# Performance work log

Hardware: AMD Instinct MI355X
Metric: run time of the kernel (lower is better)

Reference implementation:

```python
import jax, jax.numpy as jnp
import numpy as np
from jax import lax

N_NODES = 16384
N_EDGES = 262144
T = 64
F_IN = 8
H1, C1 = 12, 16          # globals H and O in the source
HID2 = H1 * C1           # 192, input to second GATConv
LSTM_H = 128
TRAIN_LEN = 32
TARGET_ID = 0
NEG_SLOPE = 0.2


def setup_inputs() -> dict:
    key = jax.random.key(0)
    ks = jax.random.split(key, 16)
    x = jax.random.normal(ks[0], (T, N_NODES, F_IN), jnp.float32)
    src = jax.random.randint(ks[1], (T, N_EDGES), 0, N_NODES)
    dst = jax.random.randint(ks[2], (T, N_EDGES), 0, N_NODES)
    dst = jnp.where(dst == src, (dst + 1) % N_NODES, dst)  # guarantee no self-loops
    edge_index = jnp.stack([src, dst], axis=1)  # (T, 2, E)
    g = lambda k, sh: jax.random.normal(k, sh, jnp.float32) * 0.1
    return {
        "x": x, "edge_index": edge_index,
        "Wl1": g(ks[3], (F_IN, H1 * C1)),
        "att_l1": g(ks[4], (1, H1, C1)), "att_r1": g(ks[5], (1, H1, C1)),
        "b1": jnp.zeros((H1 * C1,), jnp.float32),
        "Wl2": g(ks[6], (HID2, 1)),
        "att_l2": g(ks[7], (1, 1, 1)), "att_r2": g(ks[8], (1, 1, 1)),
        "b2": jnp.zeros((1,), jnp.float32),
        "Wih0": g(ks[9], (4 * LSTM_H, 1)), "Whh0": g(ks[10], (4 * LSTM_H, LSTM_H)),
        "bih0": jnp.zeros((4 * LSTM_H,), jnp.float32), "bhh0": jnp.zeros((4 * LSTM_H,), jnp.float32),
        "Wih1": g(ks[11], (4 * LSTM_H, LSTM_H)), "Whh1": g(ks[12], (4 * LSTM_H, LSTM_H)),
        "bih1": jnp.zeros((4 * LSTM_H,), jnp.float32), "bhh1": jnp.zeros((4 * LSTM_H,), jnp.float32),
        "Wlin": g(ks[13], (1, LSTM_H)), "blin": jnp.zeros((1,), jnp.float32),
    }


def _gat(x, ei, W, att_l, att_r, b, heads, outc, concat):
    N = x.shape[0]
    xl = (x @ W).reshape(N, heads, outc)              # (N,H,C)
    al = jnp.sum(xl * att_l, axis=-1)                 # (N,H)
    ar = jnp.sum(xl * att_r, axis=-1)                 # (N,H)
    loop = jnp.arange(N)
    src = jnp.concatenate([ei[0], loop])              # add self loops (inputs have none)
    dst = jnp.concatenate([ei[1], loop])
    alpha = jax.nn.leaky_relu(al[src] + ar[dst], NEG_SLOPE)  # (E+N, H)
    # segment softmax over destination neighborhoods
    amax = jax.ops.segment_max(alpha, dst, num_segments=N)
    ex = jnp.exp(alpha - amax[dst])
    alpha = ex / (jax.ops.segment_sum(ex, dst, num_segments=N)[dst] + 1e-16)
    # hardcoded per-edge-row edits from message(): s and v copies, then blend
    s = alpha.at[jnp.array([1, 2, 12, 19, 22])].set(0.0).at[jnp.array([7, 14])].set(1.0)
    v = alpha.at[jnp.array([10, 13])].set(0.5).at[jnp.array([17])].set(0.0)
    alpha = 0.8 * alpha + 0.1 * s + 0.1 * v
    out = jax.ops.segment_sum(xl[src] * alpha[:, :, None], dst, num_segments=N)  # (N,H,C)
    out = out.reshape(N, heads * outc) if concat else out.mean(axis=1)
    return out + b


def _lstm_layer(xs, Wih, Whh, bih, bhh):
    # xs: (L, B, in) -> hs: (L, B, H); torch gate order i,f,g,o
    Bsz, Hd = xs.shape[1], Whh.shape[1]
    def step(carry, xt):
        h, c = carry
        gates = xt @ Wih.T + h @ Whh.T + bih + bhh
        i, f, g, o = jnp.split(gates, 4, axis=-1)
        c = jax.nn.sigmoid(f) * c + jax.nn.sigmoid(i) * jnp.tanh(g)
        h = jax.nn.sigmoid(o) * jnp.tanh(c)
        return (h, c), h
    init = (jnp.zeros((Bsz, Hd), xs.dtype), jnp.zeros((Bsz, Hd), xs.dtype))
    _, hs = lax.scan(step, init, xs)
    return hs


def reference(x, edge_index, Wl1, att_l1, att_r1, b1, Wl2, att_l2, att_r2, b2,
              Wih0, Whh0, bih0, bhh0, Wih1, Whh1, bih1, bhh1, Wlin, blin):
    def per_t(args):
        xt, eit = args
        h = _gat(xt, eit, Wl1, att_l1, att_r1, b1, H1, C1, True)
        h = jax.nn.elu(h)
        h = _gat(h, eit, Wl2, att_l2, att_r2, b2, 1, 1, False)
        return h[:, 0]
    out = lax.map(per_t, (x, edge_index))             # (T, N) == xs_out
    series = lax.stop_gradient(out[:, TARGET_ID])     # split_sequences detaches
    idx = jnp.arange(T - TRAIN_LEN)[:, None] + jnp.arange(TRAIN_LEN)[None, :]
    ts = series[idx][:, :, None]                      # (B, L, 1), batch_first
    xs = jnp.transpose(ts, (1, 0, 2))                 # (L, B, 1)
    hs = _lstm_layer(xs, Wih0, Whh0, bih0, bhh0)
    hs = _lstm_layer(hs, Wih1, Whh1, bih1, bhh1)
    return hs[-1] @ Wlin.T + blin                     # (B, 1)
```

## Files before the change

### kernel.cpp

```cpp
#include <hip/hip_runtime.h>
#include <math.h>

#define T 64
#define NN 16384
#define NE 262144
#define FIN 8
#define H1H 12
#define C1C 16
#define HID 192
#define CAP2 95
#define SCAP 96
#define DEGCAP 127
#define LH 128
#define G4 512
#define NB 32
#define NL 32

#define DEV __device__ __forceinline__

DEV float wave_max(float v){
  #pragma unroll
  for (int m = 32; m; m >>= 1) v = fmaxf(v, __shfl_xor(v, m));
  return v;
}
DEV float wave_sum(float v){
  #pragma unroll
  for (int m = 32; m; m >>= 1) v += __shfl_xor(v, m);
  return v;
}
DEV float leaky(float x){ return x >= 0.f ? x : 0.2f * x; }
DEV float sigmoidf(float x){ return 1.f / (1.f + expf(-x)); }

DEV float apply_edit(float a, int eid){
  if (eid >= 32) return a;
  const unsigned m09 = (1u<<1)|(1u<<2)|(1u<<7)|(1u<<10)|(1u<<12)|(1u<<13)|(1u<<14)|(1u<<17)|(1u<<19)|(1u<<22);
  const unsigned mp1 = (1u<<7)|(1u<<14);
  const unsigned mp05 = (1u<<10)|(1u<<13);
  unsigned b = 1u << eid;
  float r = (m09 & b) ? 0.9f * a : a;
  if (mp1 & b) r += 0.1f;
  if (mp05 & b) r += 0.05f;
  return r;
}

__global__ __launch_bounds__(256) void k_scan0(const int* __restrict__ ei,
                                               int* __restrict__ cnt2, int* __restrict__ list2){
  long long gid = (long long)blockIdx.x * blockDim.x + threadIdx.x;
  long long e4 = gid * 4;
  int t = (int)(e4 >> 18);
  int e = (int)(e4 & (NE - 1));
  const int* dstp = ei + (size_t)t * 2 * NE + NE + e;
  int4 d = *(const int4*)dstp;
  int dd[4] = {d.x, d.y, d.z, d.w};
  #pragma unroll
  for (int q = 0; q < 4; q++){
    if (dd[q] == 0){
      int pos = atomicAdd(&cnt2[t], 1);
      if (pos < CAP2) list2[t * CAP2 + pos] = e + q;
    }
  }
}

__global__ __launch_bounds__(128) void k_build(const int* __restrict__ ei, const int* __restrict__ cnt2,
                                               const int* __restrict__ list2, int* __restrict__ scnt,
                                               int* __restrict__ Slist, int* __restrict__ slot_of,
                                               int* __restrict__ wcnt, int* __restrict__ wlist){
  int t = blockIdx.x;
  int* so = slot_of + (size_t)t * NN;
  int m = min(cnt2[t], CAP2);
  for (int i = threadIdx.x; i < m + 1; i += blockDim.x){
    int u = (i == m) ? 0 : ei[(size_t)t * 2 * NE + list2[t * CAP2 + i]];
    int old = atomicCAS(&so[u], -1, -2);
    if (old == -1){
      int s = atomicAdd(&scnt[t], 1);
      Slist[t * SCAP + s] = u;
      int w = atomicAdd(wcnt, 1);
      wlist[w] = (t << 8) | s;
      __hip_atomic_store(&so[u], s, __ATOMIC_RELAXED, __HIP_MEMORY_SCOPE_AGENT);
    }
  }
}

__global__ __launch_bounds__(256) void k_scan1(const int* __restrict__ ei, const int* __restrict__ slot_of,
                                               int* __restrict__ ecnt1, int* __restrict__ elist1){
  long long gid = (long long)blockIdx.x * blockDim.x + threadIdx.x;
  long long e4 = gid * 4;
  int t = (int)(e4 >> 18);
  int e = (int)(e4 & (NE - 1));
  const int* dstp = ei + (size_t)t * 2 * NE + NE + e;
  int4 d = *(const int4*)dstp;
  int dd[4] = {d.x, d.y, d.z, d.w};
  #pragma unroll
  for (int q = 0; q < 4; q++){
    int sl = slot_of[(size_t)t * NN + dd[q]];
    if (sl >= 0){
      int pos = atomicAdd(&ecnt1[t * SCAP + sl], 1);
      if (pos < DEGCAP) elist1[((size_t)t * SCAP + sl) * DEGCAP + pos] = e + q;
    }
  }
}

__global__ __launch_bounds__(256, 4) void k_gat1(const float* __restrict__ x, const int* __restrict__ ei,
                                             const float* __restrict__ Wl1, const float* __restrict__ attl,
                                             const float* __restrict__ attr, const float* __restrict__ b1,
                                             const int* __restrict__ wcnt, const int* __restrict__ wlist,
                                             const int* __restrict__ Slist,
                                             const int* __restrict__ ecnt1, const int* __restrict__ elist1,
                                             float* __restrict__ h1){
  int lane = threadIdx.x & 63;
  int wid = blockIdx.x * (blockDim.x >> 6) + (threadIdx.x >> 6);
  int nwaves = gridDim.x * (blockDim.x >> 6);
  int ntask = wcnt[0] * H1H;

  for (int task = wid; task < ntask; task += nwaves){
    int pi = task / H1H;
    int h = task - pi * H1H;
    int pair = wlist[pi];
    int t = pair >> 8, s = pair & 255;

    int u = Slist[t * SCAP + s];
    int deg = min(ecnt1[t * SCAP + s], DEGCAP);
    int tot = deg + 1;
    bool two = tot > 64;
    const float* xt = x + (size_t)t * NN * FIN;
    const int* srcp = ei + (size_t)t * 2 * NE;
    const int* el = elist1 + ((size_t)t * SCAP + s) * DEGCAP;

    float4 xu_a = ((const float4*)(xt + (size_t)u * FIN))[0];
    float4 xu_b = ((const float4*)(xt + (size_t)u * FIN))[1];
    float xu[FIN] = {xu_a.x, xu_a.y, xu_a.z, xu_a.w, xu_b.x, xu_b.y, xu_b.z, xu_b.w};

    bool act0 = lane < tot;
    int eid0 = 1 << 29;
    int su0 = u;
    if (lane < deg){ int e = el[lane]; eid0 = e; su0 = srcp[e]; }
    float4 xs0a = ((const float4*)(xt + (size_t)su0 * FIN))[0];
    float4 xs0b = ((const float4*)(xt + (size_t)su0 * FIN))[1];
    float xsrc0[FIN] = {xs0a.x, xs0a.y, xs0a.z, xs0a.w, xs0b.x, xs0b.y, xs0b.z, xs0b.w};

    bool act1 = false; int eid1 = 1 << 29;
    float xsrc1[FIN];
    if (two){
      int idx = 64 + lane;
      act1 = idx < tot;
      int su1 = u;
      if (idx < deg){ int e = el[idx]; eid1 = e; su1 = srcp[e]; }
      float4 xs1a = ((const float4*)(xt + (size_t)su1 * FIN))[0];
      float4 xs1b = ((const float4*)(xt + (size_t)su1 * FIN))[1];
      #pragma unroll
      for (int f = 0; f < 4; f++) xsrc1[f] = (&xs1a.x)[f];
      #pragma unroll
      for (int f = 0; f < 4; f++) xsrc1[4 + f] = (&xs1b.x)[f];
    }

    const float* Wh = Wl1 + h * C1C;
    const float* attlh = attl + h * C1C;
    const float* attrh = attr + h * C1C;

    float ar = 0.f;
    #pragma unroll
    for (int c = 0; c < C1C; c++){
      float v = 0.f;
      #pragma unroll
      for (int f = 0; f < FIN; f++) v = fmaf(xu[f], Wh[f * HID + c], v);
      ar = fmaf(v, attrh[c], ar);
    }

    float xls0[C1C];
    float al0 = 0.f;
    #pragma unroll
    for (int c = 0; c < C1C; c++){
      float v = 0.f;
      #pragma unroll
      for (int f = 0; f < FIN; f++) v = fmaf(xsrc0[f], Wh[f * HID + c], v);
      xls0[c] = v;
      al0 = fmaf(v, attlh[c], al0);
    }
    float raw0 = act0 ? leaky(al0 + ar) : -INFINITY;

    float xls1[C1C];
    float raw1 = -INFINITY;
    if (two){
      float al1 = 0.f;
      #pragma unroll
      for (int c = 0; c < C1C; c++){
        float v = 0.f;
        #pragma unroll
        for (int f = 0; f < FIN; f++) v = fmaf(xsrc1[f], Wh[f * HID + c], v);
        xls1[c] = v;
        al1 = fmaf(v, attlh[c], al1);
      }
      raw1 = act1 ? leaky(al1 + ar) : -INFINITY;
    }

    float M = wave_max(fmaxf(raw0, raw1));
    float ex0 = act0 ? expf(raw0 - M) : 0.f;
    float ex1 = act1 ? expf(raw1 - M) : 0.f;
    float S = wave_sum(ex0 + ex1);
    float den = S + 1e-16f;
    float alpha0 = apply_edit(ex0 / den, eid0);
    float alpha1 = two ? apply_edit(ex1 / den, eid1) : 0.f;

    float sum[C1C];
    #pragma unroll
    for (int c = 0; c < C1C; c++){
      sum[c] = xls0[c] * alpha0;
      if (two) sum[c] = fmaf(xls1[c], alpha1, sum[c]);
    }
    #pragma unroll
    for (int m = 32; m; m >>= 1){
      #pragma unroll
      for (int c = 0; c < C1C; c++) sum[c] += __shfl_xor(sum[c], m);
    }
    if (lane == 0){
      float* h1p = h1 + ((size_t)t * SCAP + s) * HID + h * C1C;
      #pragma unroll
      for (int c = 0; c < C1C; c++){
        float v = sum[c] + b1[h * C1C + c];
        h1p[c] = v > 0.f ? v : expm1f(v);
      }
    }
  }
}

__global__ __launch_bounds__(64) void k_gat2(const int* __restrict__ ei, const float* __restrict__ Wl2,
                                             const float* __restrict__ attl2_, const float* __restrict__ attr2_,
                                             const float* __restrict__ b2, const int* __restrict__ cnt2,
                                             const int* __restrict__ list2, const int* __restrict__ slot_of,
                                             const float* __restrict__ h1, float* __restrict__ series){
  int t = blockIdx.x; int lane = threadIdx.x;
  int deg = min(cnt2[t], CAP2);
  int tot = deg + 1;
  const int* srcp = ei + (size_t)t * 2 * NE;
  const int* so = slot_of + (size_t)t * NN;
  float attl2 = attl2_[0], attr2 = attr2_[0];
  int sl0 = so[0];
  const float* h1t = h1 + (size_t)t * SCAP * HID;

  float x0 = 0.f;
  for (int k = 0; k < HID; k++) x0 += h1t[(size_t)sl0 * HID + k] * Wl2[k];

  bool act[2]; int eid[2]; float xl2[2];
  #pragma unroll
  for (int ch = 0; ch < 2; ch++){
    int idx = ch * 64 + lane;
    act[ch] = idx < tot;
    eid[ch] = 1 << 29;
    int sl = sl0;
    if (idx < deg){ int e = list2[t * CAP2 + idx]; eid[ch] = e; sl = so[srcp[e]]; }
    float v = 0.f;
    if (act[ch]) for (int k = 0; k < HID; k++) v += h1t[(size_t)sl * HID + k] * Wl2[k];
    xl2[ch] = v;
  }
  float raw[2];
  #pragma unroll
  for (int ch = 0; ch < 2; ch++) raw[ch] = act[ch] ? leaky(attl2 * xl2[ch] + attr2 * x0) : -INFINITY;
  float M = wave_max(fmaxf(raw[0], raw[1]));
  float ex[2];
  #pragma unroll
  for (int ch = 0; ch < 2; ch++) ex[ch] = act[ch] ? expf(raw[ch] - M) : 0.f;
  float S = wave_sum(ex[0] + ex[1]);
  float den = S + 1e-16f;
  float contrib = apply_edit(ex[0] / den, eid[0]) * xl2[0] + apply_edit(ex[1] / den, eid[1]) * xl2[1];
  contrib = wave_sum(contrib);
  if (lane == 0) series[t] = contrib + b2[0];
}

#define AT_LOADR(p)    __hip_atomic_load((p), __ATOMIC_RELAXED, __HIP_MEMORY_SCOPE_AGENT)
#define AT_STORER(p,v) __hip_atomic_store((p), (v), __ATOMIC_RELAXED, __HIP_MEMORY_SCOPE_AGENT)

#define REP16(M) M(0)M(1)M(2)M(3)M(4)M(5)M(6)M(7)M(8)M(9)M(10)M(11)M(12)M(13)M(14)M(15)
#define WDECL(i) float4 w##i;
#define WLOAD(i) w##i = Wr[i];
#define WPIN(i)  asm volatile("" : "+v"(w##i.x), "+v"(w##i.y), "+v"(w##i.z), "+v"(w##i.w));
#define WFMA(i)  { float4 hv = h4b[i]; a0 = fmaf(w##i.x, hv.x, a0); a1 = fmaf(w##i.y, hv.y, a1); \
                   a2 = fmaf(w##i.z, hv.z, a2); a3 = fmaf(w##i.w, hv.w, a3); }

__global__ __launch_bounds__(512, 2) void k_lstm(const float* __restrict__ series,
    const float* __restrict__ Wih0, const float* __restrict__ Whh0,
    const float* __restrict__ bih0, const float* __restrict__ bhh0,
    const float* __restrict__ Wih1, const float* __restrict__ Whh1,
    const float* __restrict__ bih1, const float* __restrict__ bhh1,
    const float* __restrict__ Wlin, const float* __restrict__ blin,
    float* __restrict__ h0g, float* __restrict__ xpart,
    int* __restrict__ flagA, int* __restrict__ flagB, float* __restrict__ out){
  int j = threadIdx.x;
  int st = blockIdx.x >> 5;
  int b = blockIdx.x & 31;
  __shared__ float4 Wt4[16 * 512];
  __shared__ __align__(16) float h_lds[LH];
  __shared__ float c_lds[LH];
  __shared__ float gate_lds[G4];
  __shared__ float s_series[NL];
  const float4* h4b = (const float4*)h_lds;

  const float* Wsrc = (st == 0) ? Whh0 : (st == 1) ? Wih1 : Whh1;
  const float4* Wr = (const float4*)(Wsrc + (size_t)j * LH);
  REP16(WDECL)
  REP16(WLOAD)
  REP16(WPIN)
  #pragma unroll
  for (int q = 0; q < 16; q++) Wt4[q * 512 + j] = Wr[16 + q];

  if (st == 0){
    float wih = Wih0[j];
    float bsum = bih0[j] + bhh0[j];
    if (j < LH){ h_lds[j] = 0.f; c_lds[j] = 0.f; }
    if (j < NL) s_series[j] = series[b + j];
    __syncthreads();
    for (int t = 0; t < NL; t++){
      float a0 = 0.f, a1 = 0.f, a2 = 0.f, a3 = 0.f;
      REP16(WFMA)
      #pragma unroll
      for (int q = 0; q < 16; q++){
        float4 hv = h4b[16 + q];
        float4 wv = Wt4[q * 512 + j];
        a0 = fmaf(wv.x, hv.x, a0); a1 = fmaf(wv.y, hv.y, a1);
        a2 = fmaf(wv.z, hv.z, a2); a3 = fmaf(wv.w, hv.w, a3);
      }
      gate_lds[j] = fmaf(wih, s_series[t], bsum) + (a0 + a1) + (a2 + a3);
      __syncthreads();
      if (j < LH){
        float ig = sigmoidf(gate_lds[j]);
        float fg = sigmoidf(gate_lds[LH + j]);
        float gg = tanhf(gate_lds[2 * LH + j]);
        float og = sigmoidf(gate_lds[3 * LH + j]);
        float c = fg * c_lds[j] + ig * gg;
        float h = og * tanhf(c);
        c_lds[j] = c; h_lds[j] = h;
        AT_STORER(&h0g[(b * NL + t) * LH + j], h);
      }
      __syncthreads();
      if (j == 0) AT_STORER(&flagA[b], t + 1);
    }
  } else if (st == 1){
    __syncthreads();
    for (int t = 0; t < NL; t++){
      if (j == 0){
        while (AT_LOADR(&flagA[b]) < t + 1) __builtin_amdgcn_s_sleep(1);
      }
      __syncthreads();
      if (j < LH) h_lds[j] = AT_LOADR(&h0g[(b * NL + t) * LH + j]);
      __syncthreads();
      float a0 = 0.f, a1 = 0.f, a2 = 0.f, a3 = 0.f;
      REP16(WFMA)
      #pragma unroll
      for (int q = 0; q < 16; q++){
        float4 hv = h4b[16 + q];
        float4 wv = Wt4[q * 512 + j];
        a0 = fmaf(wv.x, hv.x, a0); a1 = fmaf(wv.y, hv.y, a1);
        a2 = fmaf(wv.z, hv.z, a2); a3 = fmaf(wv.w, hv.w, a3);
      }
      AT_STORER(&xpart[(b * NL + t) * G4 + j], (a0 + a1) + (a2 + a3));
      __syncthreads();
      if (j == 0) AT_STORER(&flagB[b], t + 1);
    }
  } else {
    float bsum = bih1[j] + bhh1[j];
    if (j < LH){ h_lds[j] = 0.f; c_lds[j] = 0.f; }
    __syncthreads();
    for (int t = 0; t < NL; t++){
      if (j == 0){
        while (AT_LOADR(&flagB[b]) < t + 1) __builtin_amdgcn_s_sleep(1);
      }
      __syncthreads();
      float xj = AT_LOADR(&xpart[(b * NL + t) * G4 + j]);
      float a0 = 0.f, a1 = 0.f, a2 = 0.f, a3 = 0.f;
      REP16(WFMA)
      #pragma unroll
      for (int q = 0; q < 16; q++){
        float4 hv = h4b[16 + q];
        float4 wv = Wt4[q * 512 + j];
        a0 = fmaf(wv.x, hv.x, a0); a1 = fmaf(wv.y, hv.y, a1);
        a2 = fmaf(wv.z, hv.z, a2); a3 = fmaf(wv.w, hv.w, a3);
      }
      gate_lds[j] = xj + bsum + (a0 + a1) + (a2 + a3);
      __syncthreads();
      if (j < LH){
        float ig = sigmoidf(gate_lds[j]);
        float fg = sigmoidf(gate_lds[LH + j]);
        float gg = tanhf(gate_lds[2 * LH + j]);
        float og = sigmoidf(gate_lds[3 * LH + j]);
        float c = fg * c_lds[j] + ig * gg;
        float h = og * tanhf(c);
        c_lds[j] = c; h_lds[j] = h;
      }
      __syncthreads();
    }
    if (j == 0){
      float s2 = blin[0];
      for (int k = 0; k < LH; k++) s2 += Wlin[k] * h_lds[k];
      out[b] = s2;
    }
  }
}

extern "C" void kernel_launch(void* const* d_in, const int* in_sizes, int n_in,
                              void* d_out, int out_size, void* d_ws, size_t ws_size,
                              hipStream_t stream) {
  const float* x     = (const float*)d_in[0];
  const int*   ei    = (const int*)  d_in[1];
  const float* Wl1   = (const float*)d_in[2];
  const float* attl1 = (const float*)d_in[3];
  const float* attr1 = (const float*)d_in[4];
  const float* b1    = (const float*)d_in[5];
  const float* Wl2   = (const float*)d_in[6];
  const float* attl2 = (const float*)d_in[7];
  const float* attr2 = (const float*)d_in[8];
  const float* b2    = (const float*)d_in[9];
  const float* Wih0  = (const float*)d_in[10];
  const float* Whh0  = (const float*)d_in[11];
  const float* bih0  = (const float*)d_in[12];
  const float* bhh0  = (const float*)d_in[13];
  const float* Wih1  = (const float*)d_in[14];
  const float* Whh1  = (const float*)d_in[15];
  const float* bih1  = (const float*)d_in[16];
  const float* bhh1  = (const float*)d_in[17];
  const float* Wlin  = (const float*)d_in[18];
  const float* blin  = (const float*)d_in[19];
  float* out = (float*)d_out;

  char* wsb = (char*)d_ws;
  size_t off = 0;
  auto alloc = [&](size_t bytes)->void*{
    void* p = wsb + off;
    off += (bytes + 255) & ~(size_t)255;
    return p;
  };
  int* cnt2  = (int*)alloc(T * 4);
  int* scnt  = (int*)alloc(T * 4);
  int* ecnt1 = (int*)alloc(T * SCAP * 4);
  int* flagA = (int*)alloc(NB * 4);
  int* flagB = (int*)alloc(NB * 4);
  int* wcnt  = (int*)alloc(4);
  size_t ctrl_bytes = off;
  int* slot_of = (int*)alloc((size_t)T * NN * 4);
  int* list2   = (int*)alloc((size_t)T * CAP2 * 4);
  int* Slist   = (int*)alloc((size_t)T * SCAP * 4);
  int* wlist   = (int*)alloc((size_t)T * SCAP * 4);
  int* elist1  = (int*)alloc((size_t)T * SCAP * DEGCAP * 4);
  float* h1    = (float*)alloc((size_t)T * SCAP * HID * 4);
  float* series= (float*)alloc(T * 4);
  float* h0g   = (float*)alloc((size_t)NB * NL * LH * 4);
  float* xpart = (float*)alloc((size_t)NB * NL * G4 * 4);

  hipMemsetAsync(d_ws, 0, ctrl_bytes, stream);
  hipMemsetAsync(slot_of, 0xFF, (size_t)T * NN * 4, stream);

  k_scan0<<<T * NE / 4 / 256, 256, 0, stream>>>(ei, cnt2, list2);
  k_build<<<T, 128, 0, stream>>>(ei, cnt2, list2, scnt, Slist, slot_of, wcnt, wlist);
  k_scan1<<<T * NE / 4 / 256, 256, 0, stream>>>(ei, slot_of, ecnt1, elist1);
  k_gat1<<<512, 256, 0, stream>>>(x, ei, Wl1, attl1, attr1, b1, wcnt, wlist, Slist, ecnt1, elist1, h1);
  k_gat2<<<T, 64, 0, stream>>>(ei, Wl2, attl2, attr2, b2, cnt2, list2, slot_of, h1, series);
  k_lstm<<<96, 512, 0, stream>>>(series, Wih0, Whh0, bih0, bhh0, Wih1, Whh1, bih1, bhh1,
                                 Wlin, blin, h0g, xpart, flagA, flagB, out);
}
```

Measured before the change: 495.2 us.

## Fold attention vectors into weights and aggregate raw inputs before projection in GAT1

Precomputes W·att_l and W·att_r per head in shared memory, so attention logits become 8-wide dot products on the raw input features instead of full 16-channel projections. Aggregation is now done on the 8 input features, with the weight projection applied once after the wave reduction, spread across 16 lanes. This cuts the per-edge FMA count and halves the shuffle-reduction width, at the cost of a per-block shared-memory preamble and a slightly different floating-point summation order.

Result: faster. 423.4 us (-14.5%).

```diff
diff --git a/kernel.cpp b/kernel.cpp
--- a/kernel.cpp
+++ b/kernel.cpp
@@ -100,13 +100,30 @@
   }
 }
 
-__global__ __launch_bounds__(256, 4) void k_gat1(const float* __restrict__ x, const int* __restrict__ ei,
+__global__ __launch_bounds__(256) void k_gat1(const float* __restrict__ x, const int* __restrict__ ei,
                                              const float* __restrict__ Wl1, const float* __restrict__ attl,
                                              const float* __restrict__ attr, const float* __restrict__ b1,
                                              const int* __restrict__ wcnt, const int* __restrict__ wlist,
                                              const int* __restrict__ Slist,
                                              const int* __restrict__ ecnt1, const int* __restrict__ elist1,
                                              float* __restrict__ h1){
+  __shared__ float Wsh[FIN * HID];
+  __shared__ float WAl[H1H * FIN];
+  __shared__ float WAr[H1H * FIN];
+  for (int i = threadIdx.x; i < FIN * HID; i += 256) Wsh[i] = Wl1[i];
+  __syncthreads();
+  for (int i = threadIdx.x; i < 2 * H1H * FIN; i += 256){
+    int which = i >= H1H * FIN;
+    int idx = which ? i - H1H * FIN : i;
+    int h = idx >> 3, f = idx & 7;
+    const float* av = which ? (attr + h * C1C) : (attl + h * C1C);
+    float acc = 0.f;
+    #pragma unroll
+    for (int c = 0; c < C1C; c++) acc = fmaf(Wsh[f * HID + h * C1C + c], av[c], acc);
+    (which ? WAr : WAl)[idx] = acc;
+  }
+  __syncthreads();
+
   int lane = threadIdx.x & 63;
   int wid = blockIdx.x * (blockDim.x >> 6) + (threadIdx.x >> 6);
   int nwaves = gridDim.x * (blockDim.x >> 6);
@@ -126,9 +143,14 @@
     const int* srcp = ei + (size_t)t * 2 * NE;
     const int* el = elist1 + ((size_t)t * SCAP + s) * DEGCAP;
 
-    float4 xu_a = ((const float4*)(xt + (size_t)u * FIN))[0];
-    float4 xu_b = ((const float4*)(xt + (size_t)u * FIN))[1];
-    float xu[FIN] = {xu_a.x, xu_a.y, xu_a.z, xu_a.w, xu_b.x, xu_b.y, xu_b.z, xu_b.w};
+    float ar = 0.f;
+    {
+      float4 xua = ((const float4*)(xt + (size_t)u * FIN))[0];
+      float4 xub = ((const float4*)(xt + (size_t)u * FIN))[1];
+      const float* wr = &WAr[h * FIN];
+      ar = xua.x*wr[0] + xua.y*wr[1] + xua.z*wr[2] + xua.w*wr[3]
+         + xub.x*wr[4] + xub.y*wr[5] + xub.z*wr[6] + xub.w*wr[7];
+    }
 
     bool act0 = lane < tot;
     int eid0 = 1 << 29;
@@ -139,7 +161,7 @@
     float xsrc0[FIN] = {xs0a.x, xs0a.y, xs0a.z, xs0a.w, xs0b.x, xs0b.y, xs0b.z, xs0b.w};
 
     bool act1 = false; int eid1 = 1 << 29;
-    float xsrc1[FIN];
+    float xsrc1[FIN] = {0,0,0,0,0,0,0,0};
     if (two){
       int idx = 64 + lane;
       act1 = idx < tot;
@@ -153,43 +175,15 @@
       for (int f = 0; f < 4; f++) xsrc1[4 + f] = (&xs1b.x)[f];
     }
 
-    const float* Wh = Wl1 + h * C1C;
-    const float* attlh = attl + h * C1C;
-    const float* attrh = attr + h * C1C;
-
-    float ar = 0.f;
+    const float* wl = &WAl[h * FIN];
+    float al0 = 0.f, al1 = 0.f;
     #pragma unroll
-    for (int c = 0; c < C1C; c++){
-      float v = 0.f;
-      #pragma unroll
-      for (int f = 0; f < FIN; f++) v = fmaf(xu[f], Wh[f * HID + c], v);
-      ar = fmaf(v, attrh[c], ar);
-    }
-
-    float xls0[C1C];
-    float al0 = 0.f;
-    #pragma unroll
-    for (int c = 0; c < C1C; c++){
-      float v = 0.f;
-      #pragma unroll
-      for (int f = 0; f < FIN; f++) v = fmaf(xsrc0[f], Wh[f * HID + c], v);
-      xls0[c] = v;
-      al0 = fmaf(v, attlh[c], al0);
-    }
+    for (int f = 0; f < FIN; f++) al0 = fmaf(xsrc0[f], wl[f], al0);
     float raw0 = act0 ? leaky(al0 + ar) : -INFINITY;
-
-    float xls1[C1C];
     float raw1 = -INFINITY;
     if (two){
-      float al1 = 0.f;
-      #pragma unroll
-      for (int c = 0; c < C1C; c++){
-        float v = 0.f;
-        #pragma unroll
-        for (int f = 0; f < FIN; f++) v = fmaf(xsrc1[f], Wh[f * HID + c], v);
-        xls1[c] = v;
-        al1 = fmaf(v, attlh[c], al1);
-      }
+      #pragma unroll
+      for (int f = 0; f < FIN; f++) al1 = fmaf(xsrc1[f], wl[f], al1);
       raw1 = act1 ? leaky(al1 + ar) : -INFINITY;
     }
 
@@ -201,24 +195,23 @@
     float alpha0 = apply_edit(ex0 / den, eid0);
     float alpha1 = two ? apply_edit(ex1 / den, eid1) : 0.f;
 
-    float sum[C1C];
+    float y[FIN];
     #pragma unroll
-    for (int c = 0; c < C1C; c++){
-      sum[c] = xls0[c] * alpha0;
-      if (two) sum[c] = fmaf(xls1[c], alpha1, sum[c]);
+    for (int f = 0; f < FIN; f++){
+      y[f] = xsrc0[f] * alpha0;
+      if (two) y[f] = fmaf(xsrc1[f], alpha1, y[f]);
     }
     #pragma unroll
     for (int m = 32; m; m >>= 1){
       #pragma unroll
-      for (int c = 0; c < C1C; c++) sum[c] += __shfl_xor(sum[c], m);
-    }
-    if (lane == 0){
-      float* h1p = h1 + ((size_t)t * SCAP + s) * HID + h * C1C;
-      #pragma unroll
-      for (int c = 0; c < C1C; c++){
-        float v = sum[c] + b1[h * C1C + c];
-        h1p[c] = v > 0.f ? v : expm1f(v);
-      }
+      for (int f = 0; f < FIN; f++) y[f] += __shfl_xor(y[f], m);
+    }
+
+    if (lane < C1C){
+      float v = b1[h * C1C + lane];
+      #pragma unroll
+      for (int f = 0; f < FIN; f++) v = fmaf(y[f], Wsh[f * HID + h * C1C + lane], v);
+      h1[((size_t)t * SCAP + s) * HID + h * C1C + lane] = v > 0.f ? v : expm1f(v);
     }
   }
 }
```
